# Performance work log

Hardware: AMD Instinct MI355X
Metric: run time of the kernel (lower is better)

## Reference

```python
import jax, jax.numpy as jnp
import numpy as np

D_MODEL = 1024
N_HEADS = 16
D_K = D_MODEL // N_HEADS


def setup_inputs() -> dict:
    key = jax.random.key(0)
    ks = jax.random.split(key, 11)
    B, S = 4, 2048
    inp = {
        'q': jax.random.normal(ks[0], (B, S, D_MODEL), dtype=jnp.float32),
        'k': jax.random.normal(ks[1], (B, S, D_MODEL), dtype=jnp.float32),
        'v': jax.random.normal(ks[2], (B, S, D_MODEL), dtype=jnp.float32),
    }
    scale = 1.0 / np.sqrt(D_MODEL)
    for i, name in enumerate(['Wq', 'Wk', 'Wv', 'Wo']):
        inp[name] = jax.random.normal(ks[3 + i], (D_MODEL, D_MODEL), dtype=jnp.float32) * scale
        inp['b' + name[1:]] = jnp.zeros((D_MODEL,), dtype=jnp.float32)
    return inp


def reference(q, k, v, Wq, bq, Wk, bk, Wv, bv, Wo, bo):
    B, S, _ = q.shape

    def split_heads(x):
        # [B,S,D] -> [B,H,S,d_k]
        return x.reshape(B, -1, N_HEADS, D_K).transpose(0, 2, 1, 3)

    qh = split_heads(q @ Wq.T + bq)
    kh = split_heads(k @ Wk.T + bk)
    vh = split_heads(v @ Wv.T + bv)

    scores = jnp.einsum('bhqd,bhkd->bhqk', qh, kh) / jnp.sqrt(jnp.float32(D_K))
    attn = jax.nn.softmax(scores, axis=-1)  # dropout is identity in eval / p=0
    out = jnp.einsum('bhqk,bhkd->bhqd', attn, vh)
    out = out.transpose(0, 2, 1, 3).reshape(B, -1, D_MODEL)
    return out @ Wo.T + bo
```

## Files before the change

kernel.cpp:

```cpp
#include <hip/hip_runtime.h>
#include <hip/hip_bf16.h>
#include <math.h>


#define SEQ 2048
#define NH 16
#define DKH 64
#define DM 1024
#define NB 4

#define QSCALE 0.18033688011112042f

typedef float f32x4 __attribute__((ext_vector_type(4)));
typedef __bf16 bf16x8 __attribute__((ext_vector_type(8)));
typedef __bf16 bf16x2 __attribute__((ext_vector_type(2)));

#define GLOAD16(g, l)                                                          \
    __builtin_amdgcn_global_load_lds(                                          \
        (const __attribute__((address_space(1))) void*)(g),                    \
        (__attribute__((address_space(3))) void*)(l), 16, 0, 0)

__device__ __forceinline__ float fast_exp2(float x) {
    float r;
    asm("v_exp_f32 %0, %1" : "=v"(r) : "v"(x));
    return r;
}

__global__ __launch_bounds__(256) void cvt_qkv(
    const float* __restrict__ q, const float* __restrict__ k, const float* __restrict__ v,
    __bf16* __restrict__ qb, __bf16* __restrict__ kb, __bf16* __restrict__ vb)
{
    const float* src = blockIdx.y == 0 ? q : (blockIdx.y == 1 ? k : v);
    __bf16* dst      = blockIdx.y == 0 ? qb : (blockIdx.y == 1 ? kb : vb);
    const size_t i = ((size_t)blockIdx.x * 256 + threadIdx.x) * 8;
    const float4 a = *reinterpret_cast<const float4*>(src + i);
    const float4 b = *reinterpret_cast<const float4*>(src + i + 4);
    bf16x8 o;
    o[0] = (__bf16)a.x; o[1] = (__bf16)a.y; o[2] = (__bf16)a.z; o[3] = (__bf16)a.w;
    o[4] = (__bf16)b.x; o[5] = (__bf16)b.y; o[6] = (__bf16)b.z; o[7] = (__bf16)b.w;
    *reinterpret_cast<bf16x8*>(dst + i) = o;
}

__global__ __launch_bounds__(256) void cvt_w(
    const float* __restrict__ wq, const float* __restrict__ wk,
    const float* __restrict__ wv, const float* __restrict__ wo,
    __bf16* __restrict__ oq, __bf16* __restrict__ ok,
    __bf16* __restrict__ ov, __bf16* __restrict__ oo)
{
    const int y = blockIdx.y;
    const float* src = y == 0 ? wq : (y == 1 ? wk : (y == 2 ? wv : wo));
    __bf16* dst      = y == 0 ? oq : (y == 1 ? ok : (y == 2 ? ov : oo));
    const float scale = (y == 0) ? QSCALE : 1.0f;
    const size_t i = ((size_t)blockIdx.x * 256 + threadIdx.x) * 8;
    const float4 a = *reinterpret_cast<const float4*>(src + i);
    const float4 b = *reinterpret_cast<const float4*>(src + i + 4);
    bf16x8 o;
    o[0] = (__bf16)(a.x * scale); o[1] = (__bf16)(a.y * scale);
    o[2] = (__bf16)(a.z * scale); o[3] = (__bf16)(a.w * scale);
    o[4] = (__bf16)(b.x * scale); o[5] = (__bf16)(b.y * scale);
    o[6] = (__bf16)(b.z * scale); o[7] = (__bf16)(b.w * scale);
    *reinterpret_cast<bf16x8*>(dst + i) = o;
}

template <int LAYOUT>
__global__ __launch_bounds__(256) void gemm_bf16(
    const __bf16* __restrict__ A, const __bf16* __restrict__ W,
    const float* __restrict__ bias, float bscale, void* __restrict__ outv)
{
    __shared__ __align__(16) char As[16384];
    __shared__ __align__(16) char Bs[16384];
    const int t = threadIdx.x;
    const int w = t >> 6, lane = t & 63, g = lane >> 4, ln = lane & 15;
    const int bm = blockIdx.x, bn = blockIdx.y;
    const int wr = w >> 1, wc = w & 1;

    const int srow = t >> 3;
    const int ssw  = ((t & 7) << 4) ^ ((srow & 7) << 4);

    const char* Ag = (const char*)A + (size_t)(bm * 128 + srow) * 2048 + ssw;
    const char* Wg = (const char*)W + (size_t)(bn * 128 + srow) * 2048 + ssw;

    f32x4 acc[4][4];
    #pragma unroll
    for (int i = 0; i < 4; ++i)
        #pragma unroll
        for (int j = 0; j < 4; ++j)
            #pragma unroll
            for (int e = 0; e < 4; ++e) acc[i][j][e] = 0.0f;

    for (int kb = 0; kb < 16; ++kb) {
        __syncthreads();
        #pragma unroll
        for (int c = 0; c < 4; ++c) {
            GLOAD16(Ag + kb * 128 + (size_t)c * (32 * 2048), As + c * 4096 + t * 16);
            GLOAD16(Wg + kb * 128 + (size_t)c * (32 * 2048), Bs + c * 4096 + t * 16);
        }
        __syncthreads();
        #pragma unroll
        for (int ks = 0; ks < 2; ++ks) {
            bf16x8 a[4], b[4];
            #pragma unroll
            for (int mi = 0; mi < 4; ++mi) {
                const int row = wr * 64 + mi * 16 + ln;
                a[mi] = *reinterpret_cast<const bf16x8*>(
                    As + row * 128 + (((ks * 64) + (g << 4)) ^ ((row & 7) << 4)));
            }
            #pragma unroll
            for (int ni = 0; ni < 4; ++ni) {
                const int row = wc * 64 + ni * 16 + ln;
                b[ni] = *reinterpret_cast<const bf16x8*>(
                    Bs + row * 128 + (((ks * 64) + (g << 4)) ^ ((row & 7) << 4)));
            }
            #pragma unroll
            for (int mi = 0; mi < 4; ++mi)
                #pragma unroll
                for (int ni = 0; ni < 4; ++ni)
                    acc[mi][ni] = __builtin_amdgcn_mfma_f32_16x16x32_bf16(
                        a[mi], b[ni], acc[mi][ni], 0, 0, 0);
        }
    }

    const int gm0 = bm * 128 + wr * 64, gn0 = bn * 128 + wc * 64;
    #pragma unroll
    for (int mi = 0; mi < 4; ++mi)
        #pragma unroll
        for (int ni = 0; ni < 4; ++ni) {
            const int col = gn0 + ni * 16 + ln;
            const float bs = bias[col] * bscale;
            #pragma unroll
            for (int r = 0; r < 4; ++r) {
                const int row = gm0 + mi * 16 + g * 4 + r;
                const float val = acc[mi][ni][r] + bs;
                if (LAYOUT == 0) {
                    const int bb = row >> 11, s = row & 2047;
                    const int h = col >> 6, d = col & 63;
                    ((__bf16*)outv)[(((size_t)(bb * NH + h) * SEQ) + s) * DKH + d] = (__bf16)val;
                } else {
                    ((float*)outv)[(size_t)row * DM + col] = val;
                }
            }
        }
}

__global__ __launch_bounds__(256) void transpose_v(
    const __bf16* __restrict__ Vp, __bf16* __restrict__ Vt)
{
    __shared__ __bf16 T[64][65];
    const int t = threadIdx.x, st = blockIdx.x, bh = blockIdx.y;
    const __bf16* src = Vp + ((size_t)bh * SEQ + st * 64) * DKH;
    #pragma unroll
    for (int r = 0; r < 2; ++r) {
        const int idx = r * 256 + t;
        const int s_l = idx >> 3, c8 = (idx & 7) << 3;
        const bf16x8 v8 = *reinterpret_cast<const bf16x8*>(src + s_l * DKH + c8);
        #pragma unroll
        for (int j = 0; j < 8; ++j) T[s_l][c8 + j] = v8[j];
    }
    __syncthreads();
    __bf16* dst = Vt + ((size_t)bh * DKH) * SEQ + st * 64;
    #pragma unroll
    for (int r = 0; r < 2; ++r) {
        const int idx = r * 256 + t;
        const int d = idx >> 3, s8 = (idx & 7) << 3;
        bf16x8 o;
        #pragma unroll
        for (int j = 0; j < 8; ++j) o[j] = T[s8 + j][d];
        *reinterpret_cast<bf16x8*>(dst + (size_t)d * SEQ + s8) = o;
    }
}

__global__ __launch_bounds__(256) void attn_mfma(
    const __bf16* __restrict__ Qp, const __bf16* __restrict__ Kp,
    const __bf16* __restrict__ Vt, __bf16* __restrict__ AO)
{
    __shared__ __align__(16) char Ks[16384];
    __shared__ __align__(16) char Vs[16384];
    __shared__ __align__(16) char Ps[8192];
    const int t = threadIdx.x;
    const int w = t >> 6, lane = t & 63, g = lane >> 4, ln = lane & 15;
    const int qt = blockIdx.x, bh = blockIdx.y;

    const __bf16* Qrow = Qp + ((size_t)bh * SEQ + qt * 64 + w * 16 + ln) * DKH;
    bf16x8 qf[2];
    qf[0] = *reinterpret_cast<const bf16x8*>(Qrow + g * 8);
    qf[1] = *reinterpret_cast<const bf16x8*>(Qrow + 32 + g * 8);

    const int srow = t >> 3;
    const int ssw  = ((t & 7) << 4) ^ ((srow & 7) << 4);
    const char* Kg = (const char*)Kp + ((size_t)bh * SEQ + srow) * 128 + ssw;
    const char* Vg = (const char*)Vt + ((size_t)bh * DKH + srow) * 4096 + ssw;

#define STAGE(buf, kt) do {                                                    \
        GLOAD16(Kg + (size_t)(kt) * 8192,          Ks + (buf) * 8192 + t * 16);\
        GLOAD16(Kg + (size_t)(kt) * 8192 + 4096,   Ks + (buf) * 8192 + 4096 + t * 16);\
        GLOAD16(Vg + (size_t)(kt) * 128,           Vs + (buf) * 8192 + t * 16);\
        GLOAD16(Vg + (size_t)(kt) * 128 + 32 * 4096, Vs + (buf) * 8192 + 4096 + t * 16);\
    } while (0)

    f32x4 oacc[4];
    float m = -INFINITY, l = 0.0f;
    #pragma unroll
    for (int n = 0; n < 4; ++n)
        #pragma unroll
        for (int e = 0; e < 4; ++e) oacc[n][e] = 0.0f;

    char* PsW = Ps + w * 2048;
    const int swm = (ln & 7) << 4;

    STAGE(0, 0);
    __syncthreads();

    int cur = 0;
    for (int kt = 0; kt < 32; ++kt) {
        if (kt + 1 < 32) STAGE(cur ^ 1, kt + 1);

        const char* KsC = Ks + cur * 8192;
        const char* VsC = Vs + cur * 8192;

        f32x4 sc[4];
        #pragma unroll
        for (int f = 0; f < 4; ++f)
            #pragma unroll
            for (int e = 0; e < 4; ++e) sc[f][e] = 0.0f;
        #pragma unroll
        for (int ks = 0; ks < 2; ++ks)
            #pragma unroll
            for (int f = 0; f < 4; ++f) {
                const int kr = f * 16 + ln;
                const bf16x8 kf = *reinterpret_cast<const bf16x8*>(
                    KsC + kr * 128 + (((ks * 64) + (g << 4)) ^ ((kr & 7) << 4)));
                sc[f] = __builtin_amdgcn_mfma_f32_16x16x32_bf16(kf, qf[ks], sc[f], 0, 0, 0);
            }

        bf16x8 vreg[2][4];
        #pragma unroll
        for (int ks = 0; ks < 2; ++ks)
            #pragma unroll
            for (int n = 0; n < 4; ++n) {
                const int dr = n * 16 + ln;
                vreg[ks][n] = *reinterpret_cast<const bf16x8*>(
                    VsC + dr * 128 + (((ks * 64) + (g << 4)) ^ ((dr & 7) << 4)));
            }

        float t0 = fmaxf(fmaxf(sc[0][0], sc[0][1]), fmaxf(sc[0][2], sc[0][3]));
        float t1 = fmaxf(fmaxf(sc[1][0], sc[1][1]), fmaxf(sc[1][2], sc[1][3]));
        float t2 = fmaxf(fmaxf(sc[2][0], sc[2][1]), fmaxf(sc[2][2], sc[2][3]));
        float t3 = fmaxf(fmaxf(sc[3][0], sc[3][1]), fmaxf(sc[3][2], sc[3][3]));
        float tmax = fmaxf(fmaxf(t0, t1), fmaxf(t2, t3));
        tmax = fmaxf(tmax, __shfl_xor(tmax, 16, 64));
        tmax = fmaxf(tmax, __shfl_xor(tmax, 32, 64));

        if (__any(tmax > m + 11.0f)) {
            const float mn = fmaxf(m, tmax);
            const float es = fast_exp2(m - mn);
            m = mn;
            l *= es;
            #pragma unroll
            for (int r = 0; r < 4; ++r) {
                const float er = __shfl(es, (lane & 48) + (g << 2) + r, 64);
                #pragma unroll
                for (int n = 0; n < 4; ++n) oacc[n][r] *= er;
            }
        }

        float p[4][4];
        float ss = 0.0f;
        #pragma unroll
        for (int f = 0; f < 4; ++f)
            #pragma unroll
            for (int r = 0; r < 4; ++r) {
                p[f][r] = fast_exp2(sc[f][r] - m);
                ss += p[f][r];
            }
        ss += __shfl_xor(ss, 16, 64);
        ss += __shfl_xor(ss, 32, 64);
        l += ss;

        char* prow = PsW + ln * 128;
        #pragma unroll
        for (int f = 0; f < 4; ++f) {
            bf16x2 lo, hi;
            lo[0] = (__bf16)p[f][0]; lo[1] = (__bf16)p[f][1];
            hi[0] = (__bf16)p[f][2]; hi[1] = (__bf16)p[f][3];
            const int bc = f * 32 + (g << 3);
            *reinterpret_cast<bf16x2*>(prow + ((bc) ^ swm)) = lo;
            *reinterpret_cast<bf16x2*>(prow + ((bc + 4) ^ swm)) = hi;
        }

        #pragma unroll
        for (int ks = 0; ks < 2; ++ks) {
            const bf16x8 pa = *reinterpret_cast<const bf16x8*>(
                PsW + ln * 128 + (((ks * 64) + (g << 4)) ^ swm));
            #pragma unroll
            for (int n = 0; n < 4; ++n)
                oacc[n] = __builtin_amdgcn_mfma_f32_16x16x32_bf16(
                    pa, vreg[ks][n], oacc[n], 0, 0, 0);
        }

        __syncthreads();
        cur ^= 1;
    }

    const int b = bh >> 4, h = bh & 15;
    #pragma unroll
    for (int r = 0; r < 4; ++r) {
        const float lq = __shfl(l, (lane & 48) + (g << 2) + r, 64);
        const float inv = 1.0f / lq;
        const int s = qt * 64 + w * 16 + g * 4 + r;
        __bf16* orow = AO + ((size_t)(b * SEQ + s)) * DM + h * DKH;
        #pragma unroll
        for (int n = 0; n < 4; ++n)
            orow[n * 16 + ln] = (__bf16)(oacc[n][r] * inv);
    }
#undef STAGE
}

extern "C" void kernel_launch(void* const* d_in, const int* in_sizes, int n_in,
                              void* d_out, int out_size, void* d_ws, size_t ws_size,
                              hipStream_t stream)
{
    const float* q  = (const float*)d_in[0];
    const float* k  = (const float*)d_in[1];
    const float* v  = (const float*)d_in[2];
    const float* Wq = (const float*)d_in[3];
    const float* bq = (const float*)d_in[4];
    const float* Wk = (const float*)d_in[5];
    const float* bk = (const float*)d_in[6];
    const float* Wv = (const float*)d_in[7];
    const float* bv = (const float*)d_in[8];
    const float* Wo = (const float*)d_in[9];
    const float* bo = (const float*)d_in[10];
    float* out = (float*)d_out;

    const size_t NQ = (size_t)NB * SEQ * DM;
    const size_t NW = (size_t)DM * DM;

    __bf16* qb  = (__bf16*)d_ws;
    __bf16* kb  = qb + NQ;
    __bf16* vb  = kb + NQ;
    __bf16* Wqb = vb + NQ;
    __bf16* Wkb = Wqb + NW;
    __bf16* Wvb = Wkb + NW;
    __bf16* Wob = Wvb + NW;
    __bf16* Qp  = Wob + NW;
    __bf16* Kp  = Qp + NQ;
    __bf16* Vp  = Kp + NQ;
    __bf16* VtG = qb;
    __bf16* AO  = kb;

    cvt_qkv<<<dim3(4096, 3), 256, 0, stream>>>(q, k, v, qb, kb, vb);
    cvt_w<<<dim3(512, 4), 256, 0, stream>>>(Wq, Wk, Wv, Wo, Wqb, Wkb, Wvb, Wob);

    dim3 gg(64, 8);
    gemm_bf16<0><<<gg, 256, 0, stream>>>(qb, Wqb, bq, QSCALE, Qp);
    gemm_bf16<0><<<gg, 256, 0, stream>>>(kb, Wkb, bk, 1.0f, Kp);
    gemm_bf16<0><<<gg, 256, 0, stream>>>(vb, Wvb, bv, 1.0f, Vp);
    transpose_v<<<dim3(32, 64), 256, 0, stream>>>(Vp, VtG);
    attn_mfma<<<dim3(32, 64), 256, 0, stream>>>(Qp, Kp, VtG, AO);
    gemm_bf16<1><<<gg, 256, 0, stream>>>(AO, Wob, bo, 1.0f, out);
}
```

Before: 395.9 us.

## Process two query subtiles per attention block and batch QKV projections

The attention kernel now handles 128 query rows per block (two 64-row subtiles per wave set), so each staged K/V tile and its LDS fragment reads are reused across twice as many queries. This halves the K/V global traffic and the number of blocks, at the cost of more registers and double the P scratch in LDS. The P-store swizzle is changed to write bf16x4 packets. The three Q/K/V projection GEMMs are merged into one launch via blockIdx.z, cutting launch overhead and raising occupancy for that stage.

```diff
diff --git a/kernel.cpp b/kernel.cpp
--- a/kernel.cpp
+++ b/kernel.cpp
@@ -13,7 +13,7 @@
 
 typedef float f32x4 __attribute__((ext_vector_type(4)));
 typedef __bf16 bf16x8 __attribute__((ext_vector_type(8)));
-typedef __bf16 bf16x2 __attribute__((ext_vector_type(2)));
+typedef __bf16 bf16x4 __attribute__((ext_vector_type(4)));
 
 #define GLOAD16(g, l)                                                          \
     __builtin_amdgcn_global_load_lds(                                          \
@@ -63,12 +63,11 @@
 }
 
 template <int LAYOUT>
-__global__ __launch_bounds__(256) void gemm_bf16(
+__device__ __forceinline__ void gemm_body(
     const __bf16* __restrict__ A, const __bf16* __restrict__ W,
-    const float* __restrict__ bias, float bscale, void* __restrict__ outv)
-{
-    __shared__ __align__(16) char As[16384];
-    __shared__ __align__(16) char Bs[16384];
+    const float* __restrict__ bias, float bscale, void* __restrict__ outv,
+    char* As, char* Bs)
+{
     const int t = threadIdx.x;
     const int w = t >> 6, lane = t & 63, g = lane >> 4, ln = lane & 15;
     const int bm = blockIdx.x, bn = blockIdx.y;
@@ -142,6 +141,32 @@
         }
 }
 
+__global__ __launch_bounds__(256) void gemm_qkv(
+    const __bf16* __restrict__ qb, const __bf16* __restrict__ kb, const __bf16* __restrict__ vb,
+    const __bf16* __restrict__ Wqb, const __bf16* __restrict__ Wkb, const __bf16* __restrict__ Wvb,
+    const float* __restrict__ bq, const float* __restrict__ bk, const float* __restrict__ bv,
+    __bf16* __restrict__ Qp, __bf16* __restrict__ Kp, __bf16* __restrict__ Vp)
+{
+    __shared__ __align__(16) char As[16384];
+    __shared__ __align__(16) char Bs[16384];
+    const int z = blockIdx.z;
+    const __bf16* A = z == 0 ? qb : (z == 1 ? kb : vb);
+    const __bf16* W = z == 0 ? Wqb : (z == 1 ? Wkb : Wvb);
+    const float* bias = z == 0 ? bq : (z == 1 ? bk : bv);
+    __bf16* out = z == 0 ? Qp : (z == 1 ? Kp : Vp);
+    const float bscale = z == 0 ? QSCALE : 1.0f;
+    gemm_body<0>(A, W, bias, bscale, out, As, Bs);
+}
+
+__global__ __launch_bounds__(256) void gemm_out(
+    const __bf16* __restrict__ A, const __bf16* __restrict__ W,
+    const float* __restrict__ bias, float* __restrict__ out)
+{
+    __shared__ __align__(16) char As[16384];
+    __shared__ __align__(16) char Bs[16384];
+    gemm_body<1>(A, W, bias, 1.0f, out, As, Bs);
+}
+
 __global__ __launch_bounds__(256) void transpose_v(
     const __bf16* __restrict__ Vp, __bf16* __restrict__ Vt)
 {
@@ -175,15 +200,19 @@
 {
     __shared__ __align__(16) char Ks[16384];
     __shared__ __align__(16) char Vs[16384];
-    __shared__ __align__(16) char Ps[8192];
+    __shared__ __align__(16) char Ps[16384];
     const int t = threadIdx.x;
     const int w = t >> 6, lane = t & 63, g = lane >> 4, ln = lane & 15;
     const int qt = blockIdx.x, bh = blockIdx.y;
 
-    const __bf16* Qrow = Qp + ((size_t)bh * SEQ + qt * 64 + w * 16 + ln) * DKH;
-    bf16x8 qf[2];
-    qf[0] = *reinterpret_cast<const bf16x8*>(Qrow + g * 8);
-    qf[1] = *reinterpret_cast<const bf16x8*>(Qrow + 32 + g * 8);
+    bf16x8 qf[2][2];
+    #pragma unroll
+    for (int st = 0; st < 2; ++st) {
+        const __bf16* Qrow =
+            Qp + ((size_t)bh * SEQ + qt * 128 + st * 64 + w * 16 + ln) * DKH;
+        qf[st][0] = *reinterpret_cast<const bf16x8*>(Qrow + g * 8);
+        qf[st][1] = *reinterpret_cast<const bf16x8*>(Qrow + 32 + g * 8);
+    }
 
     const int srow = t >> 3;
     const int ssw  = ((t & 7) << 4) ^ ((srow & 7) << 4);
@@ -197,15 +226,17 @@
         GLOAD16(Vg + (size_t)(kt) * 128 + 32 * 4096, Vs + (buf) * 8192 + 4096 + t * 16);\
     } while (0)
 
-    f32x4 oacc[4];
-    float m = -INFINITY, l = 0.0f;
-    #pragma unroll
-    for (int n = 0; n < 4; ++n)
-        #pragma unroll
-        for (int e = 0; e < 4; ++e) oacc[n][e] = 0.0f;
-
-    char* PsW = Ps + w * 2048;
-    const int swm = (ln & 7) << 4;
+    f32x4 oacc[2][4];
+    float m[2] = {-INFINITY, -INFINITY}, l[2] = {0.0f, 0.0f};
+    #pragma unroll
+    for (int st = 0; st < 2; ++st)
+        #pragma unroll
+        for (int n = 0; n < 4; ++n)
+            #pragma unroll
+            for (int e = 0; e < 4; ++e) oacc[st][n][e] = 0.0f;
+
+    char* PsW = Ps + w * 4096;
+    const int swp = (ln & 3) << 5;
 
     STAGE(0, 0);
     __syncthreads();
@@ -217,20 +248,31 @@
         const char* KsC = Ks + cur * 8192;
         const char* VsC = Vs + cur * 8192;
 
-        f32x4 sc[4];
-        #pragma unroll
-        for (int f = 0; f < 4; ++f)
-            #pragma unroll
-            for (int e = 0; e < 4; ++e) sc[f][e] = 0.0f;
+        bf16x8 kf[2][4];
         #pragma unroll
         for (int ks = 0; ks < 2; ++ks)
             #pragma unroll
             for (int f = 0; f < 4; ++f) {
                 const int kr = f * 16 + ln;
-                const bf16x8 kf = *reinterpret_cast<const bf16x8*>(
+                kf[ks][f] = *reinterpret_cast<const bf16x8*>(
                     KsC + kr * 128 + (((ks * 64) + (g << 4)) ^ ((kr & 7) << 4)));
-                sc[f] = __builtin_amdgcn_mfma_f32_16x16x32_bf16(kf, qf[ks], sc[f], 0, 0, 0);
-            }
+            }
+
+        f32x4 sc[2][4];
+        #pragma unroll
+        for (int st = 0; st < 2; ++st)
+            #pragma unroll
+            for (int f = 0; f < 4; ++f)
+                #pragma unroll
+                for (int e = 0; e < 4; ++e) sc[st][f][e] = 0.0f;
+        #pragma unroll
+        for (int ks = 0; ks < 2; ++ks)
+            #pragma unroll
+            for (int st = 0; st < 2; ++st)
+                #pragma unroll
+                for (int f = 0; f < 4; ++f)
+                    sc[st][f] = __builtin_amdgcn_mfma_f32_16x16x32_bf16(
+                        kf[ks][f], qf[st][ks], sc[st][f], 0, 0, 0);
 
         bf16x8 vreg[2][4];
         #pragma unroll
@@ -242,60 +284,59 @@
                     VsC + dr * 128 + (((ks * 64) + (g << 4)) ^ ((dr & 7) << 4)));
             }
 
-        float t0 = fmaxf(fmaxf(sc[0][0], sc[0][1]), fmaxf(sc[0][2], sc[0][3]));
-        float t1 = fmaxf(fmaxf(sc[1][0], sc[1][1]), fmaxf(sc[1][2], sc[1][3]));
-        float t2 = fmaxf(fmaxf(sc[2][0], sc[2][1]), fmaxf(sc[2][2], sc[2][3]));
-        float t3 = fmaxf(fmaxf(sc[3][0], sc[3][1]), fmaxf(sc[3][2], sc[3][3]));
-        float tmax = fmaxf(fmaxf(t0, t1), fmaxf(t2, t3));
-        tmax = fmaxf(tmax, __shfl_xor(tmax, 16, 64));
-        tmax = fmaxf(tmax, __shfl_xor(tmax, 32, 64));
-
-        if (__any(tmax > m + 11.0f)) {
-            const float mn = fmaxf(m, tmax);
-            const float es = fast_exp2(m - mn);
-            m = mn;
-            l *= es;
-            #pragma unroll
-            for (int r = 0; r < 4; ++r) {
-                const float er = __shfl(es, (lane & 48) + (g << 2) + r, 64);
+        #pragma unroll
+        for (int st = 0; st < 2; ++st) {
+            float t0 = fmaxf(fmaxf(sc[st][0][0], sc[st][0][1]), fmaxf(sc[st][0][2], sc[st][0][3]));
+            float t1 = fmaxf(fmaxf(sc[st][1][0], sc[st][1][1]), fmaxf(sc[st][1][2], sc[st][1][3]));
+            float t2 = fmaxf(fmaxf(sc[st][2][0], sc[st][2][1]), fmaxf(sc[st][2][2], sc[st][2][3]));
+            float t3 = fmaxf(fmaxf(sc[st][3][0], sc[st][3][1]), fmaxf(sc[st][3][2], sc[st][3][3]));
+            float tmax = fmaxf(fmaxf(t0, t1), fmaxf(t2, t3));
+            tmax = fmaxf(tmax, __shfl_xor(tmax, 16, 64));
+            tmax = fmaxf(tmax, __shfl_xor(tmax, 32, 64));
+
+            if (__any(tmax > m[st] + 11.0f)) {
+                const float mn = fmaxf(m[st], tmax);
+                const float es = fast_exp2(m[st] - mn);
+                m[st] = mn;
+                l[st] *= es;
                 #pragma unroll
-                for (int n = 0; n < 4; ++n) oacc[n][r] *= er;
-            }
+                for (int r = 0; r < 4; ++r) {
+                    const float er = __shfl(es, (lane & 48) + (g << 2) + r, 64);
+                    #pragma unroll
+                    for (int n = 0; n < 4; ++n) oacc[st][n][r] *= er;
+                }
+            }
+
+            float ss = 0.0f;
+            char* prow = PsW + st * 2048 + ln * 128;
+            #pragma unroll
+            for (int f = 0; f < 4; ++f) {
+                float p0 = fast_exp2(sc[st][f][0] - m[st]);
+                float p1 = fast_exp2(sc[st][f][1] - m[st]);
+                float p2 = fast_exp2(sc[st][f][2] - m[st]);
+                float p3 = fast_exp2(sc[st][f][3] - m[st]);
+                ss += (p0 + p1) + (p2 + p3);
+                bf16x4 pk;
+                pk[0] = (__bf16)p0; pk[1] = (__bf16)p1;
+                pk[2] = (__bf16)p2; pk[3] = (__bf16)p3;
+                *reinterpret_cast<bf16x4*>(prow + ((f * 32 + g * 8) ^ swp)) = pk;
+            }
+            ss += __shfl_xor(ss, 16, 64);
+            ss += __shfl_xor(ss, 32, 64);
+            l[st] += ss;
         }
 
-        float p[4][4];
-        float ss = 0.0f;
-        #pragma unroll
-        for (int f = 0; f < 4; ++f)
-            #pragma unroll
-            for (int r = 0; r < 4; ++r) {
-                p[f][r] = fast_exp2(sc[f][r] - m);
-                ss += p[f][r];
-            }
-        ss += __shfl_xor(ss, 16, 64);
-        ss += __shfl_xor(ss, 32, 64);
-        l += ss;
-
-        char* prow = PsW + ln * 128;
-        #pragma unroll
-        for (int f = 0; f < 4; ++f) {
-            bf16x2 lo, hi;
-            lo[0] = (__bf16)p[f][0]; lo[1] = (__bf16)p[f][1];
-            hi[0] = (__bf16)p[f][2]; hi[1] = (__bf16)p[f][3];
-            const int bc = f * 32 + (g << 3);
-            *reinterpret_cast<bf16x2*>(prow + ((bc) ^ swm)) = lo;
-            *reinterpret_cast<bf16x2*>(prow + ((bc + 4) ^ swm)) = hi;
-        }
-
-        #pragma unroll
-        for (int ks = 0; ks < 2; ++ks) {
-            const bf16x8 pa = *reinterpret_cast<const bf16x8*>(
-                PsW + ln * 128 + (((ks * 64) + (g << 4)) ^ swm));
-            #pragma unroll
-            for (int n = 0; n < 4; ++n)
-                oacc[n] = __builtin_amdgcn_mfma_f32_16x16x32_bf16(
-                    pa, vreg[ks][n], oacc[n], 0, 0, 0);
-        }
+        #pragma unroll
+        for (int st = 0; st < 2; ++st)
+            #pragma unroll
+            for (int ks = 0; ks < 2; ++ks) {
+                const bf16x8 pa = *reinterpret_cast<const bf16x8*>(
+                    PsW + st * 2048 + ln * 128 + (((ks * 64) + (g << 4)) ^ swp));
+                #pragma unroll
+                for (int n = 0; n < 4; ++n)
+                    oacc[st][n] = __builtin_amdgcn_mfma_f32_16x16x32_bf16(
+                        pa, vreg[ks][n], oacc[st][n], 0, 0, 0);
+            }
 
         __syncthreads();
         cur ^= 1;
@@ -303,15 +344,17 @@
 
     const int b = bh >> 4, h = bh & 15;
     #pragma unroll
-    for (int r = 0; r < 4; ++r) {
-        const float lq = __shfl(l, (lane & 48) + (g << 2) + r, 64);
-        const float inv = 1.0f / lq;
-        const int s = qt * 64 + w * 16 + g * 4 + r;
-        __bf16* orow = AO + ((size_t)(b * SEQ + s)) * DM + h * DKH;
-        #pragma unroll
-        for (int n = 0; n < 4; ++n)
-            orow[n * 16 + ln] = (__bf16)(oacc[n][r] * inv);
-    }
+    for (int st = 0; st < 2; ++st)
+        #pragma unroll
+        for (int r = 0; r < 4; ++r) {
+            const float lq = __shfl(l[st], (lane & 48) + (g << 2) + r, 64);
+            const float inv = 1.0f / lq;
+            const int s = qt * 128 + st * 64 + w * 16 + g * 4 + r;
+            __bf16* orow = AO + ((size_t)(b * SEQ + s)) * DM + h * DKH;
+            #pragma unroll
+            for (int n = 0; n < 4; ++n)
+                orow[n * 16 + ln] = (__bf16)(oacc[st][n][r] * inv);
+        }
 #undef STAGE
 }
 
@@ -351,11 +394,9 @@
     cvt_qkv<<<dim3(4096, 3), 256, 0, stream>>>(q, k, v, qb, kb, vb);
     cvt_w<<<dim3(512, 4), 256, 0, stream>>>(Wq, Wk, Wv, Wo, Wqb, Wkb, Wvb, Wob);
 
-    dim3 gg(64, 8);
-    gemm_bf16<0><<<gg, 256, 0, stream>>>(qb, Wqb, bq, QSCALE, Qp);
-    gemm_bf16<0><<<gg, 256, 0, stream>>>(kb, Wkb, bk, 1.0f, Kp);
-    gemm_bf16<0><<<gg, 256, 0, stream>>>(vb, Wvb, bv, 1.0f, Vp);
+    gemm_qkv<<<dim3(64, 8, 3), 256, 0, stream>>>(qb, kb, vb, Wqb, Wkb, Wvb,
+                                                 bq, bk, bv, Qp, Kp, Vp);
     transpose_v<<<dim3(32, 64), 256, 0, stream>>>(Vp, VtG);
-    attn_mfma<<<dim3(32, 64), 256, 0, stream>>>(Qp, Kp, VtG, AO);
-    gemm_bf16<1><<<gg, 256, 0, stream>>>(AO, Wob, bo, 1.0f, out);
-}
+    attn_mfma<<<dim3(16, 64), 256, 0, stream>>>(Qp, Kp, VtG, AO);
+    gemm_out<<<dim3(64, 8), 256, 0, stream>>>(AO, Wob, bo, out);
+}
```

New measurement: 385.0 us. -2.8%, faster.
